# Optimization experiments

Measured on AMD Instinct MI355X. Metric: run time of the kernel, lower is better.

Reference implementation:

```python
import jax, jax.numpy as jnp
import numpy as np

DIM_IN, DIM_OUT, DIM_INNER = 1024, 1024, 512

def setup_inputs() -> dict:
    key = jax.random.key(0)
    k1, k2, k3, k4 = jax.random.split(key, 4)
    x = jax.random.normal(k1, (4, 2048, DIM_IN), dtype=jnp.float32)
    # nn.Linear weights stored as [out, in]; init ~ U(-1/sqrt(in), 1/sqrt(in))
    w_qkv = jax.random.uniform(k2, (DIM_INNER * 3, DIM_IN), dtype=jnp.float32,
                               minval=-1.0, maxval=1.0) / np.sqrt(DIM_IN)
    w_out = jax.random.uniform(k3, (DIM_OUT, DIM_INNER), dtype=jnp.float32,
                               minval=-1.0, maxval=1.0) / np.sqrt(DIM_INNER)
    b_out = jax.random.uniform(k4, (DIM_OUT,), dtype=jnp.float32,
                               minval=-1.0, maxval=1.0) / np.sqrt(DIM_INNER)
    return {"x": x, "w_qkv": w_qkv, "w_out": w_out, "b_out": b_out}

def reference(x, w_qkv, w_out, b_out):
    scale = DIM_INNER ** -0.5
    qkv = jnp.einsum('bnd,ed->bne', x, w_qkv)  # [b, n, 3*dim_inner]
    q, k, v = jnp.split(qkv, 3, axis=-1)
    sim = jnp.einsum('bid,bjd->bij', q, k) * scale
    n = sim.shape[-1]
    causal = jnp.tril(jnp.ones((n, n), dtype=bool))  # True = keep
    sim = jnp.where(causal[None], sim, -jnp.finfo(sim.dtype).max)
    attn = jax.nn.softmax(sim, axis=-1)
    out = jnp.einsum('bij,bjd->bid', attn, v)
    return jnp.einsum('bnd,od->bno', out, w_out) + b_out
```

## Files before the change

### kernel.cpp

```cpp
#include <hip/hip_runtime.h>
#include <math.h>


typedef __attribute__((ext_vector_type(8))) short bf16x8_t;
typedef __attribute__((ext_vector_type(4))) float f32x4_t;

__device__ __forceinline__ unsigned short f2bf(float f) {
  unsigned int u = __float_as_uint(f);
  u = (u + 0x7FFFu + ((u >> 16) & 1u)) >> 16;
  return (unsigned short)u;
}
__device__ __forceinline__ float bf2f(unsigned short h) {
  return __uint_as_float(((unsigned int)h) << 16);
}

template <int N>
__device__ __forceinline__ void wait_vmcnt() {
  if constexpr (N == 0) asm volatile("s_waitcnt vmcnt(0)" ::: "memory");
  else if constexpr (N == 3) asm volatile("s_waitcnt vmcnt(3)" ::: "memory");
  else if constexpr (N == 4) asm volatile("s_waitcnt vmcnt(4)" ::: "memory");
  else if constexpr (N == 6) asm volatile("s_waitcnt vmcnt(6)" ::: "memory");
}

__global__ __launch_bounds__(256) void cvt_all(
    const float* __restrict__ x, unsigned short* __restrict__ xb, int nx,
    const float* __restrict__ w1, unsigned short* __restrict__ w1b, int n1,
    const float* __restrict__ w2, unsigned short* __restrict__ w2b, int n2) {
  const int stride = gridDim.x * blockDim.x * 4;
  const int t0 = (blockIdx.x * blockDim.x + threadIdx.x) * 4;
  for (int i = t0; i < nx; i += stride) {
    float4 f = *(const float4*)(x + i);
    ushort4 u;
    u.x = f2bf(f.x); u.y = f2bf(f.y); u.z = f2bf(f.z); u.w = f2bf(f.w);
    *(ushort4*)(xb + i) = u;
  }
  for (int i = t0; i < n1; i += stride) {
    float4 f = *(const float4*)(w1 + i);
    ushort4 u;
    u.x = f2bf(f.x); u.y = f2bf(f.y); u.z = f2bf(f.z); u.w = f2bf(f.w);
    *(ushort4*)(w1b + i) = u;
  }
  for (int i = t0; i < n2; i += stride) {
    float4 f = *(const float4*)(w2 + i);
    ushort4 u;
    u.x = f2bf(f.x); u.y = f2bf(f.y); u.z = f2bf(f.z); u.w = f2bf(f.w);
    *(ushort4*)(w2b + i) = u;
  }
}

__global__ __launch_bounds__(256) void softmax_causal(unsigned short* __restrict__ sim) {
  const int lane = threadIdx.x & 63;
  const int rowg = blockIdx.x * 4 + (threadIdx.x >> 6);
  const int i = rowg & 2047;
  unsigned short* row = sim + (size_t)rowg * 2048;
  const int nv = i + 1;
  const int tb = ((i >> 6) + 1) << 6;
  const int nc = (nv + 255) >> 8;
  const int ns = (tb + 255) >> 8;

  float v[32];
  float m = -1e30f;
#pragma unroll
  for (int c = 0; c < 8; ++c) {
    if (c < nc) {
      const int j0 = c * 256 + lane * 4;
      ushort4 u = *(const ushort4*)(row + j0);
      float f0 = bf2f(u.x), f1 = bf2f(u.y), f2 = bf2f(u.z), f3 = bf2f(u.w);
      v[c * 4 + 0] = (j0 + 0 < nv) ? f0 : -1e30f;
      v[c * 4 + 1] = (j0 + 1 < nv) ? f1 : -1e30f;
      v[c * 4 + 2] = (j0 + 2 < nv) ? f2 : -1e30f;
      v[c * 4 + 3] = (j0 + 3 < nv) ? f3 : -1e30f;
      m = fmaxf(m, fmaxf(fmaxf(v[c * 4], v[c * 4 + 1]), fmaxf(v[c * 4 + 2], v[c * 4 + 3])));
    }
  }
#pragma unroll
  for (int s = 32; s >= 1; s >>= 1) m = fmaxf(m, __shfl_xor(m, s));
  float sum = 0.f;
#pragma unroll
  for (int c = 0; c < 8; ++c) {
    if (c < nc) {
#pragma unroll
      for (int e = 0; e < 4; ++e) {
        float p = __expf(v[c * 4 + e] - m);
        v[c * 4 + e] = p;
        sum += p;
      }
    }
  }
#pragma unroll
  for (int s = 32; s >= 1; s >>= 1) sum += __shfl_xor(sum, s);
  const float inv = 1.0f / sum;
#pragma unroll
  for (int c = 0; c < 8; ++c) {
    if (c < ns) {
      const int j0 = c * 256 + lane * 4;
      ushort4 u;
      if (c < nc) {
        u.x = f2bf(v[c * 4 + 0] * inv);
        u.y = f2bf(v[c * 4 + 1] * inv);
        u.z = f2bf(v[c * 4 + 2] * inv);
        u.w = f2bf(v[c * 4 + 3] * inv);
      } else {
        u.x = u.y = u.z = u.w = 0;
      }
      *(ushort4*)(row + j0) = u;
    }
  }
}

template <int EPI, int BM, int BN, int REV, int TRI>
__global__ __launch_bounds__(256) void gemm_bt(
    const unsigned short* __restrict__ A, const unsigned short* __restrict__ B,
    int M, int N, int K, long strideA, long strideB, int klim,
    void* __restrict__ O0, void* __restrict__ O1, void* __restrict__ O2,
    const float* __restrict__ bias, float qscale) {
  int bm, bn, bz;
  if constexpr (TRI) {
    const int bid = blockIdx.x;
    bm = (int)((sqrtf(8.f * (float)bid + 1.f) - 1.f) * 0.5f);
    while ((bm + 1) * (bm + 2) / 2 <= bid) ++bm;
    while (bm * (bm + 1) / 2 > bid) --bm;
    bn = bid - bm * (bm + 1) / 2;
    bz = blockIdx.y;
  } else {
    bm = REV ? (gridDim.x - 1 - blockIdx.x) : blockIdx.x;
    bn = blockIdx.y;
    bz = blockIdx.z;
  }
  const int tid = threadIdx.x, lane = tid & 63, wave = tid >> 6;
  const int wr = wave >> 1, wc = wave & 1;
  constexpr int FM = BM / 32, FN = BN / 32;
  constexpr int AR = BM / 64, BR = BN / 64;
  constexpr int L = AR + BR;

  __shared__ alignas(16) unsigned short As[3][BM * 32];
  __shared__ alignas(16) unsigned short Bs[3][BN * 32];

  const unsigned short* Ab = A + (size_t)bz * strideA + (size_t)bm * BM * K;
  const unsigned short* Bb = B + (size_t)bz * strideB + (size_t)bn * BN * K;

  const int kmax = klim ? min(K, (bm + 1) * BM) : K;
  const int nkt = kmax >> 5;

  auto stage = [&](int buf, int kt) {
    const int loff = tid * 16;
#pragma unroll
    for (int i = 0; i < AR; ++i) {
      const int o = i * 4096 + loff;
      const int r = o >> 6;
      const int sl = ((o >> 4) & 3) ^ ((r >> 1) & 3);
      __builtin_amdgcn_global_load_lds(
          (const __attribute__((address_space(1))) void*)(
              (const char*)(Ab + (size_t)r * K) + (size_t)kt * 64 + sl * 16),
          (__attribute__((address_space(3))) void*)((char*)As[buf] + o), 16, 0, 0);
    }
#pragma unroll
    for (int i = 0; i < BR; ++i) {
      const int o = i * 4096 + loff;
      const int r = o >> 6;
      const int sl = ((o >> 4) & 3) ^ ((r >> 1) & 3);
      __builtin_amdgcn_global_load_lds(
          (const __attribute__((address_space(1))) void*)(
              (const char*)(Bb + (size_t)r * K) + (size_t)kt * 64 + sl * 16),
          (__attribute__((address_space(3))) void*)((char*)Bs[buf] + o), 16, 0, 0);
    }
  };

  f32x4_t acc[FM][FN] = {};

  stage(0, 0);
  if (nkt > 1) stage(1, 1);
  int cur = 0;
  for (int kt = 0; kt < nkt; ++kt) {
    if (kt + 1 < nkt) wait_vmcnt<L>();
    else wait_vmcnt<0>();
    __builtin_amdgcn_s_barrier();

    bf16x8_t av[FM], bv[FN];
#pragma unroll
    for (int f = 0; f < FM; ++f) {
      const int row = wr * (BM / 2) + f * 16 + (lane & 15);
      const int sp = (lane >> 4) ^ ((row >> 1) & 3);
      av[f] = *(const bf16x8_t*)((const char*)As[cur] + row * 64 + sp * 16);
    }
#pragma unroll
    for (int f = 0; f < FN; ++f) {
      const int row = wc * (BN / 2) + f * 16 + (lane & 15);
      const int sp = (lane >> 4) ^ ((row >> 1) & 3);
      bv[f] = *(const bf16x8_t*)((const char*)Bs[cur] + row * 64 + sp * 16);
    }
    if (kt + 2 < nkt) {
      int nb = cur + 2;
      if (nb >= 3) nb -= 3;
      stage(nb, kt + 2);
    }
    __builtin_amdgcn_s_setprio(1);
#pragma unroll
    for (int fi = 0; fi < FM; ++fi)
#pragma unroll
      for (int fj = 0; fj < FN; ++fj)
        acc[fi][fj] = __builtin_amdgcn_mfma_f32_16x16x32_bf16(av[fi], bv[fj], acc[fi][fj], 0, 0, 0);
    __builtin_amdgcn_s_setprio(0);
    cur = (cur + 1 == 3) ? 0 : cur + 1;
  }

#pragma unroll
  for (int fi = 0; fi < FM; ++fi) {
    const int row_l = wr * (BM / 2) + fi * 16 + ((lane >> 4) << 2);
#pragma unroll
    for (int fj = 0; fj < FN; ++fj) {
      const int col = bn * BN + wc * (BN / 2) + fj * 16 + (lane & 15);
      if constexpr (EPI == 0) {
        const int row0 = bm * BM + row_l;
        if (col < 512) {
#pragma unroll
          for (int r = 0; r < 4; ++r)
            ((unsigned short*)O0)[(size_t)(row0 + r) * 512 + col] =
                f2bf(acc[fi][fj][r] * qscale);
        } else if (col < 1024) {
#pragma unroll
          for (int r = 0; r < 4; ++r)
            ((unsigned short*)O1)[(size_t)(row0 + r) * 512 + (col - 512)] =
                f2bf(acc[fi][fj][r]);
        } else {
          const int e = col - 1024;
          const int b = row0 >> 11, n0 = row0 & 2047;
          ushort4 u;
          u.x = f2bf(acc[fi][fj][0]);
          u.y = f2bf(acc[fi][fj][1]);
          u.z = f2bf(acc[fi][fj][2]);
          u.w = f2bf(acc[fi][fj][3]);
          *(ushort4*)((unsigned short*)O2 + ((size_t)b * 512 + e) * 2048 + n0) = u;
        }
      } else {
#pragma unroll
        for (int r = 0; r < 4; ++r) {
          const int row = bm * BM + row_l + r;
          float v = acc[fi][fj][r];
          if constexpr (EPI == 1) {
            ((unsigned short*)O0)[(size_t)bz * 2048 * 2048 + (size_t)row * 2048 + col] = f2bf(v);
          } else if constexpr (EPI == 2) {
            ((unsigned short*)O0)[(size_t)bz * 2048 * 512 + (size_t)row * 512 + col] = f2bf(v);
          } else {
            ((float*)O0)[(size_t)row * 1024 + col] = v + bias[col];
          }
        }
      }
    }
  }
}

extern "C" void kernel_launch(void* const* d_in, const int* in_sizes, int n_in,
                              void* d_out, int out_size, void* d_ws, size_t ws_size,
                              hipStream_t stream) {
  const float* x = (const float*)d_in[0];
  const float* w_qkv = (const float*)d_in[1];
  const float* w_out = (const float*)d_in[2];
  const float* b_out = (const float*)d_in[3];
  float* out = (float*)d_out;

  char* ws = (char*)d_ws;
  size_t off = 0;
  auto alloc = [&](size_t bytes) {
    size_t o = off;
    off += (bytes + 255) & ~(size_t)255;
    return o;
  };
  unsigned short* xb = (unsigned short*)(ws + alloc((size_t)8192 * 1024 * 2));
  unsigned short* wqkvb = (unsigned short*)(ws + alloc((size_t)1536 * 1024 * 2));
  unsigned short* woutb = (unsigned short*)(ws + alloc((size_t)1024 * 512 * 2));
  unsigned short* qb = (unsigned short*)(ws + alloc((size_t)8192 * 512 * 2));
  unsigned short* kb = (unsigned short*)(ws + alloc((size_t)8192 * 512 * 2));
  unsigned short* vtb = (unsigned short*)(ws + alloc((size_t)8192 * 512 * 2));
  unsigned short* sim = (unsigned short*)(ws + alloc((size_t)4 * 2048 * 2048 * 2));
  unsigned short* ao = (unsigned short*)(ws + alloc((size_t)8192 * 512 * 2));

  const float scale = 1.0f / sqrtf(512.0f);

  cvt_all<<<2048, 256, 0, stream>>>(x, xb, 8192 * 1024, w_qkv, wqkvb, 1536 * 1024,
                                    w_out, woutb, 1024 * 512);

  gemm_bt<0, 128, 128, 0, 0><<<dim3(64, 12, 1), 256, 0, stream>>>(
      xb, wqkvb, 8192, 1536, 1024, 0, 0, 0, qb, kb, vtb, nullptr, scale);

  gemm_bt<1, 128, 128, 0, 1><<<dim3(136, 4, 1), 256, 0, stream>>>(
      qb, kb, 2048, 2048, 512, (long)2048 * 512, (long)2048 * 512,
      0, sim, nullptr, nullptr, nullptr, 0.f);

  softmax_causal<<<2048, 256, 0, stream>>>(sim);

  gemm_bt<2, 64, 128, 1, 0><<<dim3(32, 4, 4), 256, 0, stream>>>(
      sim, vtb, 2048, 512, 2048, (long)2048 * 2048, (long)512 * 2048,
      1, ao, nullptr, nullptr, nullptr, 0.f);

  gemm_bt<3, 128, 128, 0, 0><<<dim3(64, 8, 1), 256, 0, stream>>>(
      ao, woutb, 8192, 1024, 512, 0, 0, 0, out, nullptr, nullptr, b_out, 0.f);
}
```

Measured before the change: 128.3 us.

## Replace QKV projection GEMM with dedicated 256x256-tile 8-wave pipelined kernel

Adds a specialized QKV projection kernel that uses 256x256 output tiles, 8 waves per block and 128KB of LDS. It double-buffers A and B through swizzled direct global-to-LDS loads and interleaves the next tile's stage loads with MFMA phases under explicit barriers and priority hints. The larger tiles are meant to raise arithmetic intensity and cut global traffic for the largest GEMM. In exchange, only one block fits per CU and the grid shrinks to 192 blocks, which could underfill the GPU. The generic gemm_bt loses its QKV epilogue and unused parameters.

```diff
diff --git a/kernel.cpp b/kernel.cpp
--- a/kernel.cpp
+++ b/kernel.cpp
@@ -20,6 +20,12 @@
   else if constexpr (N == 3) asm volatile("s_waitcnt vmcnt(3)" ::: "memory");
   else if constexpr (N == 4) asm volatile("s_waitcnt vmcnt(4)" ::: "memory");
   else if constexpr (N == 6) asm volatile("s_waitcnt vmcnt(6)" ::: "memory");
+}
+__device__ __forceinline__ void bar_fence() {
+  asm volatile("s_barrier" ::: "memory");
+}
+__device__ __forceinline__ void lgkm0() {
+  asm volatile("s_waitcnt lgkmcnt(0)" ::: "memory");
 }
 
 __global__ __launch_bounds__(256) void cvt_all(
@@ -108,12 +114,171 @@
   }
 }
 
+__global__ __launch_bounds__(512, 1) void qkv_gemm8(
+    const unsigned short* __restrict__ A, const unsigned short* __restrict__ B,
+    unsigned short* __restrict__ Q, unsigned short* __restrict__ Kc,
+    unsigned short* __restrict__ VT, float qscale) {
+  constexpr int K = 1024, nkt = 16;
+  extern __shared__ char smem[];
+  const int bm = blockIdx.x, bn = blockIdx.y;
+  const int tid = threadIdx.x, lane = tid & 63, wave = tid >> 6;
+  const int wm = wave >> 2, wn = wave & 3;
+
+  const char* Ag = (const char*)(A + (size_t)bm * 256 * K);
+  const char* Bg = (const char*)(B + (size_t)bn * 256 * K);
+
+  auto stage = [&](const char* src, char* buf, int t, int h) {
+#pragma unroll
+    for (int j = 0; j < 2; ++j) {
+      const int o = h * 16384 + j * 8192 + tid * 16;
+      const int r = o >> 7;
+      const int ls = ((o >> 4) & 7) ^ (r & 7);
+      __builtin_amdgcn_global_load_lds(
+          (const __attribute__((address_space(1))) void*)(
+              src + (size_t)r * (K * 2) + t * 128 + ls * 16),
+          (__attribute__((address_space(3))) void*)(buf + o), 16, 0, 0);
+    }
+  };
+  auto rdA = [&](const char* buf, int fi, int ks) -> bf16x8_t {
+    const int row = wm * 128 + fi * 16 + (lane & 15);
+    const int sl = ((ks << 2) + (lane >> 4)) ^ (row & 7);
+    return *(const bf16x8_t*)(buf + row * 128 + sl * 16);
+  };
+  auto rdB = [&](const char* buf, int fj, int ks) -> bf16x8_t {
+    const int row = wn * 64 + fj * 16 + (lane & 15);
+    const int sl = ((ks << 2) + (lane >> 4)) ^ (row & 7);
+    return *(const bf16x8_t*)(buf + row * 128 + sl * 16);
+  };
+
+  f32x4_t acc[8][4] = {};
+  bf16x8_t bv[4][2];
+
+  stage(Bg, smem + 65536, 0, 0); stage(Bg, smem + 65536, 0, 1);
+  stage(Ag, smem, 0, 0);         stage(Ag, smem, 0, 1);
+  stage(Bg, smem + 98304, 1, 0); stage(Bg, smem + 98304, 1, 1);
+  wait_vmcnt<4>();
+  bar_fence();
+
+  for (int t = 0; t < nkt; ++t) {
+    char* Ac = smem + (t & 1) * 32768;
+    char* Bc = smem + 65536 + (t & 1) * 32768;
+    char* An = smem + ((t & 1) ^ 1) * 32768;
+    bf16x8_t av[2][2];
+
+#pragma unroll
+    for (int fj = 0; fj < 4; ++fj)
+#pragma unroll
+      for (int ks = 0; ks < 2; ++ks) bv[fj][ks] = rdB(Bc, fj, ks);
+#pragma unroll
+    for (int i = 0; i < 2; ++i)
+#pragma unroll
+      for (int ks = 0; ks < 2; ++ks) av[i][ks] = rdA(Ac, i, ks);
+    if (t + 1 < nkt) stage(Ag, An, t + 1, 0);
+    bar_fence();
+    lgkm0();
+    __builtin_amdgcn_s_setprio(1);
+#pragma unroll
+    for (int i = 0; i < 2; ++i)
+#pragma unroll
+      for (int fj = 0; fj < 4; ++fj)
+#pragma unroll
+        for (int ks = 0; ks < 2; ++ks)
+          acc[i][fj] = __builtin_amdgcn_mfma_f32_16x16x32_bf16(av[i][ks], bv[fj][ks], acc[i][fj], 0, 0, 0);
+    __builtin_amdgcn_s_setprio(0);
+    bar_fence();
+
+#pragma unroll
+    for (int i = 0; i < 2; ++i)
+#pragma unroll
+      for (int ks = 0; ks < 2; ++ks) av[i][ks] = rdA(Ac, 2 + i, ks);
+    if (t + 1 < nkt) stage(Ag, An, t + 1, 1);
+    bar_fence();
+    lgkm0();
+    __builtin_amdgcn_s_setprio(1);
+#pragma unroll
+    for (int i = 0; i < 2; ++i)
+#pragma unroll
+      for (int fj = 0; fj < 4; ++fj)
+#pragma unroll
+        for (int ks = 0; ks < 2; ++ks)
+          acc[2 + i][fj] = __builtin_amdgcn_mfma_f32_16x16x32_bf16(av[i][ks], bv[fj][ks], acc[2 + i][fj], 0, 0, 0);
+    __builtin_amdgcn_s_setprio(0);
+    bar_fence();
+
+#pragma unroll
+    for (int i = 0; i < 2; ++i)
+#pragma unroll
+      for (int ks = 0; ks < 2; ++ks) av[i][ks] = rdA(Ac, 4 + i, ks);
+    if (t + 2 < nkt) stage(Bg, Bc, t + 2, 0);
+    bar_fence();
+    lgkm0();
+    __builtin_amdgcn_s_setprio(1);
+#pragma unroll
+    for (int i = 0; i < 2; ++i)
+#pragma unroll
+      for (int fj = 0; fj < 4; ++fj)
+#pragma unroll
+        for (int ks = 0; ks < 2; ++ks)
+          acc[4 + i][fj] = __builtin_amdgcn_mfma_f32_16x16x32_bf16(av[i][ks], bv[fj][ks], acc[4 + i][fj], 0, 0, 0);
+    __builtin_amdgcn_s_setprio(0);
+    bar_fence();
+
+#pragma unroll
+    for (int i = 0; i < 2; ++i)
+#pragma unroll
+      for (int ks = 0; ks < 2; ++ks) av[i][ks] = rdA(Ac, 6 + i, ks);
+    if (t + 2 < nkt) stage(Bg, Bc, t + 2, 1);
+    if (t + 1 < nkt) {
+      if (t + 2 < nkt) wait_vmcnt<4>();
+      else wait_vmcnt<0>();
+    }
+    bar_fence();
+    lgkm0();
+    __builtin_amdgcn_s_setprio(1);
+#pragma unroll
+    for (int i = 0; i < 2; ++i)
+#pragma unroll
+      for (int fj = 0; fj < 4; ++fj)
+#pragma unroll
+        for (int ks = 0; ks < 2; ++ks)
+          acc[6 + i][fj] = __builtin_amdgcn_mfma_f32_16x16x32_bf16(av[i][ks], bv[fj][ks], acc[6 + i][fj], 0, 0, 0);
+    __builtin_amdgcn_s_setprio(0);
+    bar_fence();
+  }
+
+#pragma unroll
+  for (int fi = 0; fi < 8; ++fi) {
+    const int row0 = bm * 256 + wm * 128 + fi * 16 + ((lane >> 4) << 2);
+#pragma unroll
+    for (int fj = 0; fj < 4; ++fj) {
+      const int col = bn * 256 + wn * 64 + fj * 16 + (lane & 15);
+      if (col < 512) {
+#pragma unroll
+        for (int r = 0; r < 4; ++r)
+          Q[(size_t)(row0 + r) * 512 + col] = f2bf(acc[fi][fj][r] * qscale);
+      } else if (col < 1024) {
+#pragma unroll
+        for (int r = 0; r < 4; ++r)
+          Kc[(size_t)(row0 + r) * 512 + (col - 512)] = f2bf(acc[fi][fj][r]);
+      } else {
+        const int e = col - 1024;
+        const int b = row0 >> 11, n0 = row0 & 2047;
+        ushort4 u;
+        u.x = f2bf(acc[fi][fj][0]);
+        u.y = f2bf(acc[fi][fj][1]);
+        u.z = f2bf(acc[fi][fj][2]);
+        u.w = f2bf(acc[fi][fj][3]);
+        *(ushort4*)(VT + ((size_t)b * 512 + e) * 2048 + n0) = u;
+      }
+    }
+  }
+}
+
 template <int EPI, int BM, int BN, int REV, int TRI>
 __global__ __launch_bounds__(256) void gemm_bt(
     const unsigned short* __restrict__ A, const unsigned short* __restrict__ B,
     int M, int N, int K, long strideA, long strideB, int klim,
-    void* __restrict__ O0, void* __restrict__ O1, void* __restrict__ O2,
-    const float* __restrict__ bias, float qscale) {
+    void* __restrict__ O0, const float* __restrict__ bias) {
   int bm, bn, bz;
   if constexpr (TRI) {
     const int bid = blockIdx.x;
@@ -210,40 +375,16 @@
 #pragma unroll
     for (int fj = 0; fj < FN; ++fj) {
       const int col = bn * BN + wc * (BN / 2) + fj * 16 + (lane & 15);
-      if constexpr (EPI == 0) {
-        const int row0 = bm * BM + row_l;
-        if (col < 512) {
-#pragma unroll
-          for (int r = 0; r < 4; ++r)
-            ((unsigned short*)O0)[(size_t)(row0 + r) * 512 + col] =
-                f2bf(acc[fi][fj][r] * qscale);
-        } else if (col < 1024) {
-#pragma unroll
-          for (int r = 0; r < 4; ++r)
-            ((unsigned short*)O1)[(size_t)(row0 + r) * 512 + (col - 512)] =
-                f2bf(acc[fi][fj][r]);
+#pragma unroll
+      for (int r = 0; r < 4; ++r) {
+        const int row = bm * BM + row_l + r;
+        float v = acc[fi][fj][r];
+        if constexpr (EPI == 1) {
+          ((unsigned short*)O0)[(size_t)bz * 2048 * 2048 + (size_t)row * 2048 + col] = f2bf(v);
+        } else if constexpr (EPI == 2) {
+          ((unsigned short*)O0)[(size_t)bz * 2048 * 512 + (size_t)row * 512 + col] = f2bf(v);
         } else {
-          const int e = col - 1024;
-          const int b = row0 >> 11, n0 = row0 & 2047;
-          ushort4 u;
-          u.x = f2bf(acc[fi][fj][0]);
-          u.y = f2bf(acc[fi][fj][1]);
-          u.z = f2bf(acc[fi][fj][2]);
-          u.w = f2bf(acc[fi][fj][3]);
-          *(ushort4*)((unsigned short*)O2 + ((size_t)b * 512 + e) * 2048 + n0) = u;
-        }
-      } else {
-#pragma unroll
-        for (int r = 0; r < 4; ++r) {
-          const int row = bm * BM + row_l + r;
-          float v = acc[fi][fj][r];
-          if constexpr (EPI == 1) {
-            ((unsigned short*)O0)[(size_t)bz * 2048 * 2048 + (size_t)row * 2048 + col] = f2bf(v);
-          } else if constexpr (EPI == 2) {
-            ((unsigned short*)O0)[(size_t)bz * 2048 * 512 + (size_t)row * 512 + col] = f2bf(v);
-          } else {
-            ((float*)O0)[(size_t)row * 1024 + col] = v + bias[col];
-          }
+          ((float*)O0)[(size_t)row * 1024 + col] = v + bias[col];
         }
       }
     }
@@ -280,19 +421,18 @@
   cvt_all<<<2048, 256, 0, stream>>>(x, xb, 8192 * 1024, w_qkv, wqkvb, 1536 * 1024,
                                     w_out, woutb, 1024 * 512);
 
-  gemm_bt<0, 128, 128, 0, 0><<<dim3(64, 12, 1), 256, 0, stream>>>(
-      xb, wqkvb, 8192, 1536, 1024, 0, 0, 0, qb, kb, vtb, nullptr, scale);
+  qkv_gemm8<<<dim3(32, 6), 512, 131072, stream>>>(xb, wqkvb, qb, kb, vtb, scale);
 
   gemm_bt<1, 128, 128, 0, 1><<<dim3(136, 4, 1), 256, 0, stream>>>(
       qb, kb, 2048, 2048, 512, (long)2048 * 512, (long)2048 * 512,
-      0, sim, nullptr, nullptr, nullptr, 0.f);
+      0, sim, nullptr);
 
   softmax_causal<<<2048, 256, 0, stream>>>(sim);
 
   gemm_bt<2, 64, 128, 1, 0><<<dim3(32, 4, 4), 256, 0, stream>>>(
       sim, vtb, 2048, 512, 2048, (long)2048 * 2048, (long)512 * 2048,
-      1, ao, nullptr, nullptr, nullptr, 0.f);
+      1, ao, nullptr);
 
   gemm_bt<3, 128, 128, 0, 0><<<dim3(64, 8, 1), 256, 0, stream>>>(
-      ao, woutb, 8192, 1024, 512, 0, 0, 0, out, nullptr, nullptr, b_out, 0.f);
-}
+      ao, woutb, 8192, 1024, 512, 0, 0, 0, out, b_out);
+}
```

Result: slower. 137.2 us (+7.0%).
